# Kernel tuning notes

Measured on AMD Instinct MI355X. Metric: run time of the kernel, lower is better.

## Reference

```python
import jax, jax.numpy as jnp
import numpy as np

NUM_CLASSES = 81
TOP_K = 200
NMS_THRESH = 0.45
CONF_THRESH = 0.01
VAR = (0.1, 0.2)
BATCH = 32
NUM_PRIORS = 16384


def setup_inputs() -> dict:
    key = jax.random.key(0)
    k1, k2, k3 = jax.random.split(key, 3)
    loc_data = jax.random.normal(k1, (BATCH, NUM_PRIORS, 4), dtype=jnp.float32)
    conf_data = jax.random.uniform(k2, (BATCH * NUM_PRIORS, NUM_CLASSES), dtype=jnp.float32)
    prior_data = jax.random.uniform(k3, (NUM_PRIORS, 4), dtype=jnp.float32)
    return {"loc_data": loc_data, "conf_data": conf_data, "prior_data": prior_data}


def _decode(loc, priors):
    # SSD box decode: priors are (cx, cy, w, h); loc are encoded offsets.
    cxcy = priors[:, :2] + loc[:, :2] * VAR[0] * priors[:, 2:]
    wh = priors[:, 2:] * jnp.exp(loc[:, 2:] * VAR[1])
    mins = cxcy - 0.5 * wh          # (xmin, ymin)
    maxs = mins + wh                # (xmax, ymax)
    return jnp.concatenate([mins, maxs], axis=1)  # [P, 4]


def _pairwise_iou(boxes):
    # boxes: [K, 4] corner format -> IoU matrix [K, K]
    area = jnp.clip(boxes[:, 2] - boxes[:, 0], 0.0) * jnp.clip(boxes[:, 3] - boxes[:, 1], 0.0)
    lt = jnp.maximum(boxes[:, None, :2], boxes[None, :, :2])
    rb = jnp.minimum(boxes[:, None, 2:], boxes[None, :, 2:])
    wh = jnp.clip(rb - lt, 0.0)
    inter = wh[..., 0] * wh[..., 1]
    union = area[:, None] + area[None, :] - inter
    return inter / jnp.maximum(union, 1e-12)


def _nms_class(boxes, scores):
    # boxes: [P, 4], scores: [P] for one (image, class).
    # Original: threshold by conf, then greedy NMS over the top_k highest-scoring
    # candidates (ssd.pytorch nms considers only top_k candidates).
    s = jnp.where(scores > CONF_THRESH, scores, -jnp.inf)
    top_s, top_i = jax.lax.top_k(s, TOP_K)          # sorted descending
    cand = boxes[top_i]                              # [K, 4]
    iou = _pairwise_iou(cand)                        # [K, K]
    ok = top_s > -jnp.inf

    def body(j, keep):
        # if candidate j is kept, suppress all later candidates with IoU > thresh
        sup = (jnp.arange(TOP_K) > j) & keep[j] & (iou[j] > NMS_THRESH)
        return keep & ~sup

    keep = jax.lax.fori_loop(0, TOP_K, body, ok)
    # compact kept detections to the front (stable), matching output[i, cl, :count]
    order = jnp.argsort(~keep)                       # stable: kept (False) first
    rows = jnp.concatenate([top_s[:, None], cand], axis=1)[order]  # [K, 5]
    return jnp.where(keep[order][:, None], rows, 0.0)


def reference(loc_data, conf_data, prior_data):
    num = loc_data.shape[0]
    P = prior_data.shape[0]
    # [B, C, P] like conf_preds = view(num, P, C).transpose(2, 1)
    conf = conf_data.reshape(num, P, NUM_CLASSES).transpose(0, 2, 1)

    def per_image(loc_i, conf_i):
        boxes = _decode(loc_i, prior_data)           # [P, 4]
        # classes 1..C-1 (class 0 = background stays all-zero)
        fg = jax.vmap(lambda sc: _nms_class(boxes, sc))(conf_i[1:])  # [C-1, K, 5]
        bg = jnp.zeros((1, TOP_K, 5), fg.dtype)
        return jnp.concatenate([bg, fg], axis=0)     # [C, K, 5]

    # Note: the original's final rank-based fill_(0) operates on an advanced-
    # indexing copy in PyTorch and is a no-op, so the output is returned as-is.
    return jax.vmap(per_image)(loc_data, conf)       # [B, C, K, 5]
```

## Files before the change

### kernel.cpp

```cpp
#include <hip/hip_runtime.h>
#include <stdint.h>

#pragma clang fp contract(off)

#define NUM_CLASSES 81
#define TOP_K 200
#define BATCH 32
#define NUM_PRIORS 16384
#define CAP 512
#define CONF_T 0.01f
#define NMS_T 0.45f
#define PIVOT_S 0.97827148f
#define NTASK (BATCH * (NUM_CLASSES - 1))
#define QCAP 1536
#define ROWS_PER_BLK 256
#define FILTER_BLOCKS 2048
#define NB 1024

typedef unsigned long long u64;
typedef unsigned int u32;

__device__ __forceinline__ float exp_ref(float x) {
#pragma clang fp contract(off)
    return (float)exp((double)x);
}

struct SharedBlk {
    u64 keys[CAP];
    union {
        u64 sup[TOP_K][4];
        struct { u32 bcnt[NB]; u32 flag; } srt;
    } a;
    union {
        struct { float box[TOP_K][5]; float score[TOP_K]; } bx;
        u64 keys2[CAP];
    } b;
    u64 keep[4];
    u32 wsum[4];
    u32 acc;
    u32 ctr;
};

__device__ int count_pass(const float* cbase, u64 pivot, int tid, int lane, u32* s_acc) {
#pragma clang fp contract(off)
    __syncthreads();
    if (tid == 0) *s_acc = 0u;
    __syncthreads();
    u32 ph = (u32)(pivot >> 32), pl = (u32)pivot;
    u32 c = 0;
    for (int j = 0; j < 64; ++j) {
        int p = tid + (j << 8);
        float s = cbase[(size_t)p * NUM_CLASSES];
        bool valid = s > CONF_T;
        u32 bt = valid ? __float_as_uint(s) : 0u;
        u32 il = ~(u32)p;
        c += (valid && ((bt > ph) || ((bt == ph) && (il > pl)))) ? 1u : 0u;
    }
    for (int off = 32; off > 0; off >>= 1) c += __shfl_down(c, off, 64);
    if (lane == 0) atomicAdd(s_acc, c);
    __syncthreads();
    return (int)*s_acc;
}

__device__ int gather_pass(const float* cbase, u64 pivot, int tid, int lane,
                           u64* s_keys, u32* s_acc, u32* s_ctr) {
#pragma clang fp contract(off)
    __syncthreads();
    if (tid == 0) { *s_acc = 0u; *s_ctr = 0u; }
    for (int q = tid; q < CAP; q += 256) s_keys[q] = 0ull;
    __syncthreads();
    u32 ph = (u32)(pivot >> 32), pl = (u32)pivot;
    u32 cnt = 0;
    for (int j = 0; j < 64; ++j) {
        int p = tid + (j << 8);
        float s = cbase[(size_t)p * NUM_CLASSES];
        bool valid = s > CONF_T;
        u32 bt = valid ? __float_as_uint(s) : 0u;
        u32 il = ~(u32)p;
        bool pred = valid && ((bt > ph) || ((bt == ph) && (il > pl)));
        cnt += pred ? 1u : 0u;
        u64 mk = __ballot(pred);
        u32 off = 0;
        if (lane == 0 && mk) off = atomicAdd(s_ctr, (u32)__popcll(mk));
        off = __shfl(off, 0, 64);
        if (pred) {
            u32 pos = off + (u32)__popcll(mk & ((1ull << lane) - 1ull));
            if (pos < CAP) s_keys[pos] = ((u64)bt << 32) | il;
        }
    }
    for (int off2 = 32; off2 > 0; off2 >>= 1) cnt += __shfl_down(cnt, off2, 64);
    if (lane == 0) atomicAdd(s_acc, cnt);
    __syncthreads();
    return (int)*s_acc;
}

__device__ __forceinline__ void bitonic_desc(u64* k, int tid) {
    for (int k2 = 2; k2 <= CAP; k2 <<= 1) {
        for (int jj = k2 >> 1; jj > 0; jj >>= 1) {
            __syncthreads();
            for (int i = tid; i < CAP; i += 256) {
                int ixj = i ^ jj;
                if (ixj > i) {
                    u64 a = k[i], bb = k[ixj];
                    bool up = ((i & k2) == 0);
                    if (up ? (a < bb) : (a > bb)) { k[i] = bb; k[ixj] = a; }
                }
            }
        }
    }
    __syncthreads();
}

__global__ __launch_bounds__(256) void filter_kernel(
    const float4* __restrict__ conf4,
    u32* __restrict__ counts, u64* __restrict__ keys)
{
#pragma clang fp contract(off)
    __shared__ u64 qkey[QCAP];
    __shared__ u32 tcnt[80];
    __shared__ u32 qn;

    const int tid = threadIdx.x;
    const int lane = tid & 63;
    const int bid = blockIdx.x;
    const int img = bid & 31;
    const int chunk = bid >> 5;
    const int row0 = img * NUM_PRIORS + chunk * ROWS_PER_BLK;
    const int base4 = row0 * NUM_CLASSES / 4;

    if (tid == 0) qn = 0u;
    if (tid < 80) tcnt[tid] = 0u;
    __syncthreads();

    #pragma unroll 4
    for (int it = 0; it < 21; ++it) {
        int le4 = tid + it * 256;
        if (it == 20 && tid >= 64) break;
        float4 v = conf4[base4 + le4];
        float vv[4] = {v.x, v.y, v.z, v.w};

        bool h0, h1, h2, h3;
        {
            u32 le0 = (u32)(le4 * 4);
            u32 r0 = le0 / NUM_CLASSES;
            u32 c0 = le0 - r0 * NUM_CLASSES;
            h0 = (vv[0] > PIVOT_S) && (c0 != 0u);
            u32 c1 = c0 + 1u, c2 = c0 + 2u, c3 = c0 + 3u;
            h1 = (vv[1] > PIVOT_S) && (c1 != 81u);
            h2 = (vv[2] > PIVOT_S) && (c2 != 81u) && (c2 != 162u);
            h3 = (vv[3] > PIVOT_S) && (c3 != 81u) && (c3 != 162u);
        }
        u32 hc = (h0?1u:0u) + (h1?1u:0u) + (h2?1u:0u) + (h3?1u:0u);

        u64 b1 = __ballot(hc >= 1u);
        if (b1) {
            u64 b2 = __ballot(hc >= 2u);
            u64 b3 = __ballot(hc >= 3u);
            u64 b4 = __ballot(hc >= 4u);
            u32 tot = (u32)(__popcll(b1) + __popcll(b2) + __popcll(b3) + __popcll(b4));
            u32 base = 0;
            if (lane == 0) base = atomicAdd(&qn, tot);
            base = __shfl(base, 0, 64);
            if (hc) {
                u64 lt = (1ull << lane) - 1ull;
                u32 off = base + (u32)(__popcll(b1 & lt) + __popcll(b2 & lt)
                                     + __popcll(b3 & lt) + __popcll(b4 & lt));
                #pragma unroll
                for (int j = 0; j < 4; ++j) {
                    bool hj = (j == 0) ? h0 : (j == 1) ? h1 : (j == 2) ? h2 : h3;
                    if (hj) {
                        u32 le = (u32)(le4 * 4 + j);
                        u32 lrow = le / NUM_CLASSES;
                        u32 c = le - lrow * NUM_CLASSES;
                        u32 p = (u32)(chunk * ROWS_PER_BLK) + lrow;
                        u64 key = ((u64)__float_as_uint(vv[j]) << 32)
                                | ((u64)(16383u - p) << 7) | (u64)(c - 1u);
                        if (off < QCAP) qkey[off] = key;
                        ++off;
                    }
                }
            }
        }
    }
    __syncthreads();

    u32 qtotal = qn;
    u32 qvalid = qtotal < QCAP ? qtotal : QCAP;

    for (u32 q = tid; q < qvalid; q += 256)
        atomicAdd(&tcnt[(u32)(qkey[q] & 0x7Full)], 1u);
    __syncthreads();

    if (tid < 80) {
        u32 n = tcnt[tid];
        u32 base = 0;
        if (n) base = atomicAdd(&counts[img * 80 + tid], n);
        tcnt[tid] = base;
    }
    __syncthreads();

    for (u32 q = tid; q < qvalid; q += 256) {
        u64 k = qkey[q];
        u32 t = (u32)(k & 0x7Full);
        u32 slot = atomicAdd(&tcnt[t], 1u);
        if (slot < CAP) keys[(size_t)(img * 80 + t) * CAP + slot] = k;
    }
    if (qtotal > QCAP) {
        if (tid < 80) atomicAdd(&counts[img * 80 + tid], 0x01000000u);
    }
}

__global__ __launch_bounds__(256) void nms_kernel(
    const float* __restrict__ loc_data,
    const float* __restrict__ conf_data,
    const float* __restrict__ prior_data,
    const u32* __restrict__ counts,
    const u64* __restrict__ gkeys,
    float* __restrict__ out,
    int use_ws)
{
#pragma clang fp contract(off)
    __shared__ SharedBlk sh;
    const int tid = threadIdx.x;
    const int lane = tid & 63;
    const int wv = tid >> 6;
    const int b = blockIdx.x;
    const int img = b / 80;
    const int r = b - img * 80;
    const int cl = r + 1;
    const int task = img * 80 + r;

    const float* cbase = conf_data + (size_t)img * NUM_PRIORS * NUM_CLASSES + cl;

    int m = -1;
    bool fast = false;
    if (use_ws) {
        u32 cnt = counts[task];
        if (cnt >= TOP_K && cnt <= CAP) {
            const u64* src = gkeys + (size_t)task * CAP;
            for (int q = tid; q < CAP; q += 256) {
                u64 k = 0ull;
                if (q < (int)cnt) {
                    u64 kw = src[q];
                    u32 p = 16383u - ((u32)(kw >> 7) & 0x3FFFu);
                    k = (kw & 0xFFFFFFFF00000000ull) | (u64)(u32)(~p);
                }
                sh.keys[q] = k;
            }
            m = (int)cnt;
            fast = true;
        }
    }
    if (m < 0) {
        u64 pivot = ((u64)__float_as_uint(PIVOT_S) << 32) | 0xFFFFFFFFull;
        m = gather_pass(cbase, pivot, tid, lane, sh.keys, &sh.acc, &sh.ctr);
        if (m < TOP_K || m > CAP) {
            const u32 B001 = __float_as_uint(CONF_T);
            int nvalid = count_pass(cbase, ((u64)B001 << 32) | 0xFFFFFFFFull, tid, lane, &sh.acc);
            if (nvalid <= CAP) {
                pivot = 0ull;
            } else {
                u64 lo = ((u64)B001 << 32) | 0xFFFFFFFFull;
                u64 hi = ~0ull;
                for (int it = 0; it < 64; ++it) {
                    u64 mid = lo + ((hi - lo) >> 1);
                    int c = count_pass(cbase, mid, tid, lane, &sh.acc);
                    if (c >= TOP_K && c <= CAP) { pivot = mid; break; }
                    if (c > CAP) lo = mid; else hi = mid;
                }
            }
            m = gather_pass(cbase, pivot, tid, lane, sh.keys, &sh.acc, &sh.ctr);
        }
    }
    const int nk = m < TOP_K ? m : TOP_K;

    bool in_k2 = false;
    if (fast) {
        for (int i = tid; i < NB; i += 256) sh.a.srt.bcnt[i] = 0u;
        if (tid == 0) sh.a.srt.flag = 0u;
        __syncthreads();
        const u32 LOB = __float_as_uint(PIVOT_S);
        for (int q = tid; q < m; q += 256) {
            u32 sb = (u32)(sh.keys[q] >> 32);
            u32 bi = (sb - LOB - 1u) >> 9;
            if (bi > (u32)(NB - 1)) bi = (u32)(NB - 1);
            atomicAdd(&sh.a.srt.bcnt[(u32)(NB - 1) - bi], 1u);
        }
        __syncthreads();
        u32 c0 = sh.a.srt.bcnt[tid * 4 + 0];
        u32 c1 = sh.a.srt.bcnt[tid * 4 + 1];
        u32 c2 = sh.a.srt.bcnt[tid * 4 + 2];
        u32 c3 = sh.a.srt.bcnt[tid * 4 + 3];
        u32 s = c0 + c1 + c2 + c3;
        u32 inc = s;
        #pragma unroll
        for (int o = 1; o < 64; o <<= 1) {
            u32 t = __shfl_up(inc, o, 64);
            if (lane >= o) inc += t;
        }
        if (lane == 63) sh.wsum[wv] = inc;
        __syncthreads();
        u32 wpre = 0;
        #pragma unroll
        for (int w = 0; w < 4; ++w) wpre += (w < wv) ? sh.wsum[w] : 0u;
        u32 ex = wpre + inc - s;
        sh.a.srt.bcnt[tid * 4 + 0] = ex;
        sh.a.srt.bcnt[tid * 4 + 1] = ex + c0;
        sh.a.srt.bcnt[tid * 4 + 2] = ex + c0 + c1;
        sh.a.srt.bcnt[tid * 4 + 3] = ex + c0 + c1 + c2;
        __syncthreads();
        for (int q = tid; q < m; q += 256) {
            u64 k = sh.keys[q];
            u32 sb = (u32)(k >> 32);
            u32 bi = (sb - LOB - 1u) >> 9;
            if (bi > (u32)(NB - 1)) bi = (u32)(NB - 1);
            u32 slot = atomicAdd(&sh.a.srt.bcnt[(u32)(NB - 1) - bi], 1u);
            sh.b.keys2[slot] = k;
        }
        __syncthreads();
        for (int bb = tid; bb < NB; bb += 256) {
            u32 e = sh.a.srt.bcnt[bb];
            u32 st = bb ? sh.a.srt.bcnt[bb - 1] : 0u;
            if ((int)(e - st) > 32) { sh.a.srt.flag = 1u; continue; }
            for (u32 i = st + 1; i < e; ++i) {
                u64 x = sh.b.keys2[i];
                int j = (int)i - 1;
                while (j >= (int)st && sh.b.keys2[j] < x) {
                    sh.b.keys2[j + 1] = sh.b.keys2[j];
                    --j;
                }
                sh.b.keys2[j + 1] = x;
            }
        }
        __syncthreads();
        u32 fl = sh.a.srt.flag;
        if (!fl) in_k2 = true;
        else bitonic_desc(sh.keys, tid);
    } else {
        bitonic_desc(sh.keys, tid);
    }

    {
        u64 key = 0ull;
        if (tid < nk) key = in_k2 ? sh.b.keys2[tid] : sh.keys[tid];
        float4 lc, pr;
        int p = 0;
        if (tid < nk) {
            p = (int)(~(u32)key);
            lc = *(const float4*)(loc_data + ((size_t)img * NUM_PRIORS + p) * 4);
            pr = *(const float4*)(prior_data + (size_t)p * 4);
        }
        __syncthreads();
        if (tid < nk) {
            float sc = __uint_as_float((u32)(key >> 32));
            float cx = pr.x + (lc.x * 0.1f) * pr.z;
            float cy = pr.y + (lc.y * 0.1f) * pr.w;
            float w  = pr.z * exp_ref(lc.z * 0.2f);
            float h  = pr.w * exp_ref(lc.w * 0.2f);
            float x1 = cx - 0.5f * w;
            float y1 = cy - 0.5f * h;
            float x2 = x1 + w;
            float y2 = y1 + h;
            sh.b.bx.box[tid][0] = x1; sh.b.bx.box[tid][1] = y1;
            sh.b.bx.box[tid][2] = x2; sh.b.bx.box[tid][3] = y2;
            sh.b.bx.box[tid][4] = fmaxf(x2 - x1, 0.0f) * fmaxf(y2 - y1, 0.0f);
            sh.b.bx.score[tid] = sc;
        }
    }
    __syncthreads();

    {
        const double M45 = (double)0.45f + 0x1p-26;
        u64 m0 = 0ull, m1 = 0ull, m2 = 0ull, m3 = 0ull;
        if (tid < nk) {
            const float bx0 = sh.b.bx.box[tid][0], by0 = sh.b.bx.box[tid][1];
            const float bx1 = sh.b.bx.box[tid][2], by1 = sh.b.bx.box[tid][3];
            const float aj  = sh.b.bx.box[tid][4];
            #pragma unroll
            for (int c = 0; c < 4; ++c) {
                u64 mm = 0ull;
                int klo = tid + 1 > (c << 6) ? tid + 1 : (c << 6);
                int khi = nk < ((c + 1) << 6) ? nk : ((c + 1) << 6);
                for (int k = klo; k < khi; ++k) {
                    float ltx = fmaxf(bx0, sh.b.bx.box[k][0]);
                    float lty = fmaxf(by0, sh.b.bx.box[k][1]);
                    float rbx = fminf(bx1, sh.b.bx.box[k][2]);
                    float rby = fminf(by1, sh.b.bx.box[k][3]);
                    float wx = fmaxf(rbx - ltx, 0.0f);
                    float wy = fmaxf(rby - lty, 0.0f);
                    float inter = wx * wy;
                    float uni = (aj + sh.b.bx.box[k][4]) - inter;
                    float denom = fmaxf(uni, 1e-12f);
                    if ((double)inter > M45 * (double)denom) mm |= 1ull << (k & 63);
                }
                if (c == 0) m0 = mm; else if (c == 1) m1 = mm;
                else if (c == 2) m2 = mm; else m3 = mm;
            }
        }
        if (tid < TOP_K) {
            sh.a.sup[tid][0] = m0; sh.a.sup[tid][1] = m1;
            sh.a.sup[tid][2] = m2; sh.a.sup[tid][3] = m3;
        }
    }
    __syncthreads();

    if (wv == 0) {
        u64 kws[4];
        #pragma unroll
        for (int w = 0; w < 4; ++w) {
            int rem = nk - (w << 6);
            kws[w] = rem >= 64 ? ~0ull : (rem <= 0 ? 0ull : ((1ull << rem) - 1ull));
        }
        for (int c = 0; c < 4; ++c) {
            int row = (c << 6) + lane;
            u64 myrow = (row < TOP_K) ? sh.a.sup[row][c] : 0ull;
            u64 kw = kws[c];
            u64 nz = __ballot(myrow != 0ull);
            u64 t = kw & nz;
            while (t) {
                int j = __ffsll(t) - 1;
                u64 rj = __shfl(myrow, j, 64);
                kw &= ~rj;
                t &= ~(1ull << j);
                t &= kw;
            }
            kws[c] = kw;
            for (int w2 = c + 1; w2 < 4; ++w2) {
                u64 contrib = (row < TOP_K && ((kw >> lane) & 1ull)) ? sh.a.sup[row][w2] : 0ull;
                #pragma unroll
                for (int off = 32; off > 0; off >>= 1) contrib |= __shfl_xor(contrib, off, 64);
                kws[w2] &= ~contrib;
            }
        }
        if (lane == 0) {
            sh.keep[0] = kws[0]; sh.keep[1] = kws[1];
            sh.keep[2] = kws[2]; sh.keep[3] = kws[3];
        }
    }
    __syncthreads();

    if (tid < nk) {
        int w = tid >> 6, rr = tid & 63;
        u64 kwv = sh.keep[w];
        if ((kwv >> rr) & 1ull) {
            int pos = __popcll(kwv & ((1ull << rr) - 1ull));
            for (int q = 0; q < w; ++q) pos += __popcll(sh.keep[q]);
            float* o = out + (((size_t)img * NUM_CLASSES + cl) * TOP_K + pos) * 5;
            o[0] = sh.b.bx.score[tid];
            o[1] = sh.b.bx.box[tid][0];
            o[2] = sh.b.bx.box[tid][1];
            o[3] = sh.b.bx.box[tid][2];
            o[4] = sh.b.bx.box[tid][3];
        }
    }
}

extern "C" void kernel_launch(void* const* d_in, const int* in_sizes, int n_in,
                              void* d_out, int out_size, void* d_ws, size_t ws_size,
                              hipStream_t stream) {
    const float* loc   = (const float*)d_in[0];
    const float* conf  = (const float*)d_in[1];
    const float* prior = (const float*)d_in[2];
    float* out = (float*)d_out;

    hipMemsetAsync(d_out, 0, (size_t)out_size * sizeof(float), stream);

    const size_t need = 65536 + (size_t)NTASK * CAP * 8;
    const int use_ws = (ws_size >= need) ? 1 : 0;

    u32* counts = (u32*)d_ws;
    u64* keys   = (u64*)((char*)d_ws + 65536);

    if (use_ws) {
        hipMemsetAsync(d_ws, 0, NTASK * sizeof(u32), stream);
        filter_kernel<<<FILTER_BLOCKS, 256, 0, stream>>>((const float4*)conf, counts, keys);
    }
    nms_kernel<<<NTASK, 256, 0, stream>>>(loc, conf, prior,
                                          use_ws ? counts : nullptr,
                                          use_ws ? keys : nullptr,
                                          out, use_ws);
}
```

Measured before the change: 120.4 us.

## Stage NMS output in LDS, write full slices, drop output memset

The kernel now builds each (image, class) output slice in shared memory, zero-filled with the kept detections compacted in, and writes the whole 1000-float slice with coalesced float4 stores. The background class slice is zeroed by the r==0 block, so the separate hipMemsetAsync over the whole output is removed. Boxes are stored as float4 with the area recomputed on the fly, and the IoU loop uses wave-uniform bounds with a per-lane predicate to reduce divergence. In exchange every block writes its full slice, adds extra syncs and LDS zeroing, and does redundant IoU work on masked lanes.

```diff
diff --git a/kernel.cpp b/kernel.cpp
--- a/kernel.cpp
+++ b/kernel.cpp
@@ -26,13 +26,16 @@
 }
 
 struct SharedBlk {
-    u64 keys[CAP];
+    union {
+        u64 keys[CAP];
+        float4 outstage4[250];
+    } k;
     union {
         u64 sup[TOP_K][4];
         struct { u32 bcnt[NB]; u32 flag; } srt;
     } a;
     union {
-        struct { float box[TOP_K][5]; float score[TOP_K]; } bx;
+        struct { float4 box4[TOP_K]; float score[TOP_K]; } bx;
         u64 keys2[CAP];
     } b;
     u64 keep[4];
@@ -245,7 +248,7 @@
                     u32 p = 16383u - ((u32)(kw >> 7) & 0x3FFFu);
                     k = (kw & 0xFFFFFFFF00000000ull) | (u64)(u32)(~p);
                 }
-                sh.keys[q] = k;
+                sh.k.keys[q] = k;
             }
             m = (int)cnt;
             fast = true;
@@ -253,7 +256,7 @@
     }
     if (m < 0) {
         u64 pivot = ((u64)__float_as_uint(PIVOT_S) << 32) | 0xFFFFFFFFull;
-        m = gather_pass(cbase, pivot, tid, lane, sh.keys, &sh.acc, &sh.ctr);
+        m = gather_pass(cbase, pivot, tid, lane, sh.k.keys, &sh.acc, &sh.ctr);
         if (m < TOP_K || m > CAP) {
             const u32 B001 = __float_as_uint(CONF_T);
             int nvalid = count_pass(cbase, ((u64)B001 << 32) | 0xFFFFFFFFull, tid, lane, &sh.acc);
@@ -269,7 +272,7 @@
                     if (c > CAP) lo = mid; else hi = mid;
                 }
             }
-            m = gather_pass(cbase, pivot, tid, lane, sh.keys, &sh.acc, &sh.ctr);
+            m = gather_pass(cbase, pivot, tid, lane, sh.k.keys, &sh.acc, &sh.ctr);
         }
     }
     const int nk = m < TOP_K ? m : TOP_K;
@@ -281,7 +284,7 @@
         __syncthreads();
         const u32 LOB = __float_as_uint(PIVOT_S);
         for (int q = tid; q < m; q += 256) {
-            u32 sb = (u32)(sh.keys[q] >> 32);
+            u32 sb = (u32)(sh.k.keys[q] >> 32);
             u32 bi = (sb - LOB - 1u) >> 9;
             if (bi > (u32)(NB - 1)) bi = (u32)(NB - 1);
             atomicAdd(&sh.a.srt.bcnt[(u32)(NB - 1) - bi], 1u);
@@ -310,7 +313,7 @@
         sh.a.srt.bcnt[tid * 4 + 3] = ex + c0 + c1 + c2;
         __syncthreads();
         for (int q = tid; q < m; q += 256) {
-            u64 k = sh.keys[q];
+            u64 k = sh.k.keys[q];
             u32 sb = (u32)(k >> 32);
             u32 bi = (sb - LOB - 1u) >> 9;
             if (bi > (u32)(NB - 1)) bi = (u32)(NB - 1);
@@ -335,18 +338,17 @@
         __syncthreads();
         u32 fl = sh.a.srt.flag;
         if (!fl) in_k2 = true;
-        else bitonic_desc(sh.keys, tid);
+        else bitonic_desc(sh.k.keys, tid);
     } else {
-        bitonic_desc(sh.keys, tid);
+        bitonic_desc(sh.k.keys, tid);
     }
 
     {
         u64 key = 0ull;
-        if (tid < nk) key = in_k2 ? sh.b.keys2[tid] : sh.keys[tid];
+        if (tid < nk) key = in_k2 ? sh.b.keys2[tid] : sh.k.keys[tid];
         float4 lc, pr;
-        int p = 0;
         if (tid < nk) {
-            p = (int)(~(u32)key);
+            int p = (int)(~(u32)key);
             lc = *(const float4*)(loc_data + ((size_t)img * NUM_PRIORS + p) * 4);
             pr = *(const float4*)(prior_data + (size_t)p * 4);
         }
@@ -361,9 +363,7 @@
             float y1 = cy - 0.5f * h;
             float x2 = x1 + w;
             float y2 = y1 + h;
-            sh.b.bx.box[tid][0] = x1; sh.b.bx.box[tid][1] = y1;
-            sh.b.bx.box[tid][2] = x2; sh.b.bx.box[tid][3] = y2;
-            sh.b.bx.box[tid][4] = fmaxf(x2 - x1, 0.0f) * fmaxf(y2 - y1, 0.0f);
+            sh.b.bx.box4[tid] = make_float4(x1, y1, x2, y2);
             sh.b.bx.score[tid] = sc;
         }
     }
@@ -371,31 +371,36 @@
 
     {
         const double M45 = (double)0.45f + 0x1p-26;
+        float4 mybox = make_float4(0.f, 0.f, 0.f, 0.f);
+        float aj = 0.f;
+        if (tid < nk) {
+            mybox = sh.b.bx.box4[tid];
+            aj = fmaxf(mybox.z - mybox.x, 0.0f) * fmaxf(mybox.w - mybox.y, 0.0f);
+        }
         u64 m0 = 0ull, m1 = 0ull, m2 = 0ull, m3 = 0ull;
-        if (tid < nk) {
-            const float bx0 = sh.b.bx.box[tid][0], by0 = sh.b.bx.box[tid][1];
-            const float bx1 = sh.b.bx.box[tid][2], by1 = sh.b.bx.box[tid][3];
-            const float aj  = sh.b.bx.box[tid][4];
-            #pragma unroll
-            for (int c = 0; c < 4; ++c) {
-                u64 mm = 0ull;
-                int klo = tid + 1 > (c << 6) ? tid + 1 : (c << 6);
-                int khi = nk < ((c + 1) << 6) ? nk : ((c + 1) << 6);
-                for (int k = klo; k < khi; ++k) {
-                    float ltx = fmaxf(bx0, sh.b.bx.box[k][0]);
-                    float lty = fmaxf(by0, sh.b.bx.box[k][1]);
-                    float rbx = fminf(bx1, sh.b.bx.box[k][2]);
-                    float rby = fminf(by1, sh.b.bx.box[k][3]);
-                    float wx = fmaxf(rbx - ltx, 0.0f);
-                    float wy = fmaxf(rby - lty, 0.0f);
-                    float inter = wx * wy;
-                    float uni = (aj + sh.b.bx.box[k][4]) - inter;
-                    float denom = fmaxf(uni, 1e-12f);
-                    if ((double)inter > M45 * (double)denom) mm |= 1ull << (k & 63);
-                }
-                if (c == 0) m0 = mm; else if (c == 1) m1 = mm;
-                else if (c == 2) m2 = mm; else m3 = mm;
-            }
+        const int kloW = (wv << 6) + 1;
+        #pragma unroll
+        for (int c = 0; c < 4; ++c) {
+            u64 mm = 0ull;
+            int khi = ((c + 1) << 6); if (khi > nk) khi = nk;
+            int klo = (c << 6); if (klo < kloW) klo = kloW;
+            for (int k = klo; k < khi; ++k) {
+                float4 bk = sh.b.bx.box4[k];
+                float ak = fmaxf(bk.z - bk.x, 0.0f) * fmaxf(bk.w - bk.y, 0.0f);
+                float ltx = fmaxf(mybox.x, bk.x);
+                float lty = fmaxf(mybox.y, bk.y);
+                float rbx = fminf(mybox.z, bk.z);
+                float rby = fminf(mybox.w, bk.w);
+                float wx = fmaxf(rbx - ltx, 0.0f);
+                float wy = fmaxf(rby - lty, 0.0f);
+                float inter = wx * wy;
+                float uni = (aj + ak) - inter;
+                float denom = fmaxf(uni, 1e-12f);
+                if (tid < k && tid < nk && (double)inter > M45 * (double)denom)
+                    mm |= 1ull << (k & 63);
+            }
+            if (c == 0) m0 = mm; else if (c == 1) m1 = mm;
+            else if (c == 2) m2 = mm; else m3 = mm;
         }
         if (tid < TOP_K) {
             sh.a.sup[tid][0] = m0; sh.a.sup[tid][1] = m1;
@@ -439,18 +444,30 @@
     }
     __syncthreads();
 
-    if (tid < nk) {
-        int w = tid >> 6, rr = tid & 63;
-        u64 kwv = sh.keep[w];
-        if ((kwv >> rr) & 1ull) {
-            int pos = __popcll(kwv & ((1ull << rr) - 1ull));
-            for (int q = 0; q < w; ++q) pos += __popcll(sh.keep[q]);
-            float* o = out + (((size_t)img * NUM_CLASSES + cl) * TOP_K + pos) * 5;
-            o[0] = sh.b.bx.score[tid];
-            o[1] = sh.b.bx.box[tid][0];
-            o[2] = sh.b.bx.box[tid][1];
-            o[3] = sh.b.bx.box[tid][2];
-            o[4] = sh.b.bx.box[tid][3];
+    {
+        float* os = (float*)sh.k.outstage4;
+        for (int i = tid; i < (TOP_K * 5) / 2; i += 256) ((u64*)os)[i] = 0ull;
+        __syncthreads();
+        if (tid < nk) {
+            int w = tid >> 6, rr = tid & 63;
+            u64 kwv = sh.keep[w];
+            if ((kwv >> rr) & 1ull) {
+                int pos = __popcll(kwv & ((1ull << rr) - 1ull));
+                for (int q = 0; q < w; ++q) pos += __popcll(sh.keep[q]);
+                float4 bx = sh.b.bx.box4[tid];
+                os[pos * 5 + 0] = sh.b.bx.score[tid];
+                os[pos * 5 + 1] = bx.x;
+                os[pos * 5 + 2] = bx.y;
+                os[pos * 5 + 3] = bx.z;
+                os[pos * 5 + 4] = bx.w;
+            }
+        }
+        __syncthreads();
+        float4* oslice = (float4*)(out + (((size_t)img * NUM_CLASSES + cl) * TOP_K) * 5);
+        if (tid < 250) oslice[tid] = sh.k.outstage4[tid];
+        if (r == 0) {
+            float4* bg = (float4*)(out + (((size_t)img * NUM_CLASSES) * TOP_K) * 5);
+            if (tid < 250) bg[tid] = make_float4(0.f, 0.f, 0.f, 0.f);
         }
     }
 }
@@ -463,8 +480,6 @@
     const float* prior = (const float*)d_in[2];
     float* out = (float*)d_out;
 
-    hipMemsetAsync(d_out, 0, (size_t)out_size * sizeof(float), stream);
-
     const size_t need = 65536 + (size_t)NTASK * CAP * 8;
     const int use_ws = (ws_size >= need) ? 1 : 0;
 
```

After: 132.6 us, median of 2. 10.2% more time.
